# Kernel tuning notes

Measured on AMD Instinct MI355X. Metric: run time of the kernel, lower is better.

Reference implementation:

```python
import jax, jax.numpy as jnp
import numpy as np

HIDDEN = 1024
NUM_HEADS = 4
HEAD_DIM = HIDDEN // NUM_HEADS
SCALE = HEAD_DIM ** -0.5
EPS = 1e-5


def setup_inputs() -> dict:
    key = jax.random.key(0)
    ks = jax.random.split(key, 8)
    B, S, D = 4, 2048, HIDDEN
    x = jax.random.normal(ks[0], (B, S, D), dtype=jnp.float32)
    attention_mask = jnp.ones((B, S), dtype=jnp.int32)
    init = 1.0 / np.sqrt(D)
    Wq = jax.random.uniform(ks[1], (D, D), jnp.float32, -init, init)
    Wk = jax.random.uniform(ks[2], (D, D), jnp.float32, -init, init)
    Wv = jax.random.uniform(ks[3], (D, D), jnp.float32, -init, init)
    Wo = jax.random.uniform(ks[4], (D, D), jnp.float32, -init, init)
    bo = jax.random.uniform(ks[5], (D,), jnp.float32, -init, init)
    gamma = jnp.ones((D,), dtype=jnp.float32)
    beta = jnp.zeros((D,), dtype=jnp.float32)
    return {"x": x, "attention_mask": attention_mask, "Wq": Wq, "Wk": Wk,
            "Wv": Wv, "Wo": Wo, "bo": bo, "gamma": gamma, "beta": beta}


def reference(x, attention_mask, Wq, Wk, Wv, Wo, bo, gamma, beta):
    # Linear layers: y = x @ W^T (torch nn.Linear convention), no bias for q/k/v
    q = jnp.einsum('bsd,ed->bse', x, Wq)
    k = jnp.einsum('bsd,ed->bse', x, Wk)
    v = jnp.einsum('bsd,ed->bse', x, Wv)
    # Full-width attention (module never splits heads), scale = head_dim^-0.5
    scores = jnp.einsum('bqd,bkd->bqk', q, k) * SCALE  # [B,S,S]
    mask = attention_mask[:, None, :]  # [B,1,S]
    scores = jnp.where(mask == 0, jnp.float32(-1e9), scores)
    attn = jax.nn.softmax(scores, axis=-1)
    ctx = jnp.einsum('bqk,bkd->bqd', attn, v)
    out = jnp.einsum('bsd,ed->bse', ctx, Wo) + bo
    # residual + LayerNorm
    h = out + x
    mu = jnp.mean(h, axis=-1, keepdims=True)
    var = jnp.mean(jnp.square(h - mu), axis=-1, keepdims=True)
    return (h - mu) * jax.lax.rsqrt(var + EPS) * gamma + beta
```

## Files before the change

### kernel.cpp

```cpp
#include <hip/hip_runtime.h>

typedef __bf16 bf16;
typedef __bf16 bf16x8 __attribute__((ext_vector_type(8)));
typedef __bf16 bf16x4 __attribute__((ext_vector_type(4)));
typedef float floatx4 __attribute__((ext_vector_type(4)));

#define HIDDEN 1024
#define SEQ 2048
#define BATCH 4
#define ATT_SCALE 0.0625f
#define LN_EPS 1e-5f
#define WW (HIDDEN * HIDDEN)

__device__ __forceinline__ void gload_lds16(const void* g, void* l) {
    __builtin_amdgcn_global_load_lds(
        (const __attribute__((address_space(1))) unsigned int*)g,
        (__attribute__((address_space(3))) unsigned int*)l, 16, 0, 0);
}

#define GBAR() asm volatile("s_barrier" ::: "memory")
#define LGKM0() do { asm volatile("s_waitcnt lgkmcnt(0)" ::: "memory"); \
                     __builtin_amdgcn_sched_barrier(0); } while (0)
#define VMC(N) asm volatile("s_waitcnt vmcnt(" #N ")" ::: "memory")
#define MFMA(a, b, c) __builtin_amdgcn_mfma_f32_16x16x32_bf16(a, b, c, 0, 0, 0)

__global__ void cvt_f32_bf16(const float* __restrict__ in, bf16* __restrict__ out, int n4) {
    int i = blockIdx.x * blockDim.x + threadIdx.x;
    if (i >= n4) return;
    float4 v = ((const float4*)in)[i];
    bf16x4 o;
    o[0] = (bf16)v.x; o[1] = (bf16)v.y; o[2] = (bf16)v.z; o[3] = (bf16)v.w;
    ((bf16x4*)out)[i] = o;
}

__global__ void transpose_w3(const float* __restrict__ s0, const float* __restrict__ s1,
                             const float* __restrict__ s2,
                             bf16* __restrict__ d0p, bf16* __restrict__ d1p, bf16* __restrict__ d2p) {
    const float* in = (blockIdx.z == 0) ? s0 : (blockIdx.z == 1) ? s1 : s2;
    bf16* out = (blockIdx.z == 0) ? d0p : (blockIdx.z == 1) ? d1p : d2p;
    __shared__ __attribute__((aligned(16))) bf16 tile[64][72];
    const int d0 = blockIdx.x * 64;
    const int f0 = blockIdx.y * 64;
    const int t = threadIdx.x;
    const int r = t >> 4;
    const int c = (t & 15) * 4;
#pragma unroll
    for (int i = 0; i < 4; ++i) {
        float4 v = *(const float4*)&in[(long)(f0 + r + i * 16) * HIDDEN + d0 + c];
        bf16x4 b;
        b[0] = (bf16)v.x; b[1] = (bf16)v.y; b[2] = (bf16)v.z; b[3] = (bf16)v.w;
        *(bf16x4*)&tile[r + i * 16][c] = b;
    }
    __syncthreads();
#pragma unroll
    for (int i = 0; i < 4; ++i) {
        const int dr = r + i * 16;
        bf16x4 o;
#pragma unroll
        for (int j = 0; j < 4; ++j) o[j] = tile[c + j][dr];
        *(bf16x4*)&out[(long)(d0 + dr) * HIDDEN + f0 + c] = o;
    }
}

template <int MODE>
__global__ __launch_bounds__(512, 2)
void gemm8p(const bf16* A, const bf16* Bw, void* __restrict__ Cout,
            int lda, int ldb, int ldc, int K, float scale,
            long sA, long sB, long sC, int zmod) {
    __shared__ __attribute__((aligned(16))) char lds[131072];

    const int gx = gridDim.x;
    const int nblk = gx * gridDim.y;
    const int bid = blockIdx.y * gx + blockIdx.x;
    const int cpx = nblk >> 3;
    const int sbid = (nblk & 7) ? bid : (bid & 7) * cpx + (bid >> 3);
    const int bx = sbid % gx, by = sbid / gx;

    const int z = blockIdx.z;
    const int mat = z % zmod, ks = z / zmod;
    const char* Ab = (const char*)(A + (long)mat * sA + (long)ks * K);
    const char* Bb = (const char*)(Bw + (long)mat * sB + (long)ks * K);
    const long lda2 = lda * 2L, ldb2 = ldb * 2L;

    const int t = threadIdx.x;
    const int lane = t & 63;
    const int w = t >> 6;
    const int wm = w >> 2;
    const int wn = w & 3;
    const int l15 = lane & 15;
    const int l4 = lane >> 4;

    const int row0 = by * 256;
    const int col0 = bx * 256;

    const int sc = ((((t & 3) - ((t >> 3) & 3)) & 3) << 4);
    const char* aS[2];
    const char* bS[2];
#pragma unroll
    for (int uu = 0; uu < 2; ++uu) {
        aS[uu] = Ab + (long)(row0 + uu * 128 + (t >> 2)) * lda2 + sc;
        bS[uu] = Bb + (long)(col0 + uu * 128 + (t >> 2)) * ldb2 + sc;
    }

    auto STAGE = [&](char* dstu, const char* const* sp, long koff) {
        gload_lds16(sp[0] + koff, dstu + t * 16);
        gload_lds16(sp[1] + koff, dstu + 8192 + t * 16);
    };

    floatx4 acc[8][4] = {};
    const int nk = K / 64;

    STAGE(lds + 0,     aS, 0);
    STAGE(lds + 16384, bS, 0);
    STAGE(lds + 32768, aS, 64);
    STAGE(lds + 49152, bS, 64);
    VMC(4);
    GBAR();

    for (int tt = 0; tt < nk; ++tt) {
        const char* cb = lds + (tt & 1) * 65536;
        char* nb = lds + ((tt & 1) ^ 1) * 65536;
        const long nko = (long)((tt + 1 < nk) ? tt + 1 : nk - 1) * 128;

        auto RDA = [&](int kk, int m) {
            int lr = wm * 128 + m * 16 + l15;
            return *(const bf16x8*)(cb + kk * 32768 + lr * 64 + ((((lr >> 1) + l4) & 3) << 4));
        };
        auto RDB = [&](int kk, int n) {
            int lr = wn * 64 + n * 16 + l15;
            return *(const bf16x8*)(cb + 16384 + kk * 32768 + lr * 64 + ((((lr >> 1) + l4) & 3) << 4));
        };

        bf16x8 a[4], b0[4], b1[4];

#pragma unroll
        for (int m = 0; m < 4; ++m) a[m] = RDA(0, m);
#pragma unroll
        for (int n = 0; n < 4; ++n) b0[n] = RDB(0, n);
        STAGE(nb + 0, aS, nko);
        GBAR();
        LGKM0();
        __builtin_amdgcn_s_setprio(1);
#pragma unroll
        for (int m = 0; m < 4; ++m)
#pragma unroll
            for (int n = 0; n < 4; ++n) acc[m][n] = MFMA(a[m], b0[n], acc[m][n]);
        __builtin_amdgcn_s_setprio(0);
        GBAR();

#pragma unroll
        for (int m = 0; m < 4; ++m) a[m] = RDA(0, 4 + m);
        STAGE(nb + 16384, bS, nko);
        GBAR();
        LGKM0();
        __builtin_amdgcn_s_setprio(1);
#pragma unroll
        for (int m = 0; m < 4; ++m)
#pragma unroll
            for (int n = 0; n < 4; ++n) acc[4 + m][n] = MFMA(a[m], b0[n], acc[4 + m][n]);
        __builtin_amdgcn_s_setprio(0);
        VMC(4);
        GBAR();

#pragma unroll
        for (int m = 0; m < 4; ++m) a[m] = RDA(1, m);
#pragma unroll
        for (int n = 0; n < 4; ++n) b1[n] = RDB(1, n);
        STAGE(nb + 32768, aS, nko + 64);
        GBAR();
        LGKM0();
        __builtin_amdgcn_s_setprio(1);
#pragma unroll
        for (int m = 0; m < 4; ++m)
#pragma unroll
            for (int n = 0; n < 4; ++n) acc[m][n] = MFMA(a[m], b1[n], acc[m][n]);
        __builtin_amdgcn_s_setprio(0);
        GBAR();

#pragma unroll
        for (int m = 0; m < 4; ++m) a[m] = RDA(1, 4 + m);
        STAGE(nb + 49152, bS, nko + 64);
        GBAR();
        LGKM0();
        __builtin_amdgcn_s_setprio(1);
#pragma unroll
        for (int m = 0; m < 4; ++m)
#pragma unroll
            for (int n = 0; n < 4; ++n) acc[4 + m][n] = MFMA(a[m], b1[n], acc[4 + m][n]);
        __builtin_amdgcn_s_setprio(0);
        VMC(4);
        GBAR();
    }
    VMC(0);

    const int rq = l4 * 4;
    if constexpr (MODE == 0) {
        bf16* C = ((bf16*)Cout) + (long)z * sC;
#pragma unroll
        for (int m = 0; m < 8; ++m)
#pragma unroll
            for (int i = 0; i < 4; ++i) {
                long gr = row0 + wm * 128 + m * 16 + rq + i;
#pragma unroll
                for (int n = 0; n < 4; ++n) {
                    int gc = col0 + wn * 64 + n * 16 + l15;
                    C[gr * ldc + gc] = (bf16)(acc[m][n][i] * scale);
                }
            }
    } else {
        float* C = (float*)Cout + (long)z * sC;
#pragma unroll
        for (int m = 0; m < 8; ++m)
#pragma unroll
            for (int i = 0; i < 4; ++i) {
                long gr = row0 + wm * 128 + m * 16 + rq + i;
#pragma unroll
                for (int n = 0; n < 4; ++n) {
                    int gc = col0 + wn * 64 + n * 16 + l15;
                    C[gr * ldc + gc] = acc[m][n][i];
                }
            }
    }
}

__global__ void reduce_wgc(const float* __restrict__ p, bf16* __restrict__ out) {
    int i = blockIdx.x * blockDim.x + threadIdx.x;
    int e = i * 4;
    int mat = e >> 20;
    int local = e & (WW - 1);
    float4 s = *(const float4*)(p + (long)mat * WW + local);
#pragma unroll
    for (int ksp = 1; ksp < 4; ++ksp) {
        float4 a = *(const float4*)(p + (long)(ksp * 2 + mat) * WW + local);
        s.x += a.x; s.y += a.y; s.z += a.z; s.w += a.w;
    }
    bf16x4 o;
    o[0] = (bf16)s.x; o[1] = (bf16)s.y; o[2] = (bf16)s.z; o[3] = (bf16)s.w;
    *(bf16x4*)&out[e] = o;
}

__global__ void softmax_rows(bf16* __restrict__ S, const int* __restrict__ mask) {
    const int b = blockIdx.y;
    const int row = blockIdx.x;
    bf16* srow = S + ((long)b * SEQ + row) * SEQ;
    const int* mrow = mask + b * SEQ;
    const int t = threadIdx.x;

    bf16x8 sv = *(const bf16x8*)&srow[t * 8];
    int4 m0 = ((const int4*)mrow)[t * 2];
    int4 m1 = ((const int4*)mrow)[t * 2 + 1];
    int mk[8] = {m0.x, m0.y, m0.z, m0.w, m1.x, m1.y, m1.z, m1.w};

    float v[8];
    float mx = -1e30f;
#pragma unroll
    for (int j = 0; j < 8; ++j) {
        float s = (float)sv[j];
        if (mk[j] == 0) s = -1e9f;
        v[j] = s;
        mx = fmaxf(mx, s);
    }
    __shared__ float redm[4], reds[4];
#pragma unroll
    for (int off = 32; off > 0; off >>= 1) mx = fmaxf(mx, __shfl_down(mx, off));
    if ((t & 63) == 0) redm[t >> 6] = mx;
    __syncthreads();
    mx = fmaxf(fmaxf(redm[0], redm[1]), fmaxf(redm[2], redm[3]));

    float sum = 0.f;
#pragma unroll
    for (int j = 0; j < 8; ++j) {
        v[j] = __expf(v[j] - mx);
        sum += v[j];
    }
#pragma unroll
    for (int off = 32; off > 0; off >>= 1) sum += __shfl_down(sum, off);
    if ((t & 63) == 0) reds[t >> 6] = sum;
    __syncthreads();
    sum = reds[0] + reds[1] + reds[2] + reds[3];
    float inv = 1.0f / sum;

    bf16x8 o;
#pragma unroll
    for (int j = 0; j < 8; ++j) o[j] = (bf16)(v[j] * inv);
    *(bf16x8*)&srow[t * 8] = o;
}

__global__ void transpose_v(const bf16* __restrict__ yv, bf16* __restrict__ out) {
    __shared__ __attribute__((aligned(16))) bf16 tile[64][72];
    const int z = blockIdx.z;
    const bf16* ib = yv + (long)z * SEQ * 2048 + 1024;
    bf16* ob = out + (long)z * SEQ * HIDDEN;
    const int d0 = blockIdx.x * 64;
    const int s0 = blockIdx.y * 64;
    const int t = threadIdx.x;
    const int r = t >> 4;
    const int c = (t & 15) * 4;
#pragma unroll
    for (int i = 0; i < 4; ++i) {
        bf16x4 v = *(const bf16x4*)&ib[(long)(s0 + r + i * 16) * 2048 + d0 + c];
        *(bf16x4*)&tile[r + i * 16][c] = v;
    }
    __syncthreads();
#pragma unroll
    for (int i = 0; i < 4; ++i) {
        const int dr = r + i * 16;
        bf16x4 o;
#pragma unroll
        for (int j = 0; j < 4; ++j) o[j] = tile[c + j][dr];
        *(bf16x4*)&ob[(long)(d0 + dr) * SEQ + s0 + c] = o;
    }
}

__global__ void layernorm_out(const bf16* __restrict__ pp, const float* __restrict__ x,
                              const float* __restrict__ bo, const float* __restrict__ gamma,
                              const float* __restrict__ beta, float* __restrict__ out) {
    const long row = blockIdx.x;
    const int b = (int)(row >> 11);
    const int s = (int)(row & 2047);
    const bf16* r0 = pp + ((long)b * SEQ + s) * HIDDEN;
    const bf16* r1 = r0 + 4L * SEQ * HIDDEN;
    const int t = threadIdx.x;

    bf16x4 a0 = ((const bf16x4*)r0)[t];
    bf16x4 a1 = ((const bf16x4*)r1)[t];
    float4 xv = ((const float4*)(x + row * HIDDEN))[t];
    float4 bv = ((const float4*)bo)[t];
    float4 v;
    v.x = (float)a0[0] + (float)a1[0] + bv.x + xv.x;
    v.y = (float)a0[1] + (float)a1[1] + bv.y + xv.y;
    v.z = (float)a0[2] + (float)a1[2] + bv.z + xv.z;
    v.w = (float)a0[3] + (float)a1[3] + bv.w + xv.w;

    float ssum = v.x + v.y + v.z + v.w;
    float sq = v.x * v.x + v.y * v.y + v.z * v.z + v.w * v.w;
    __shared__ float rs[4], rq[4];
#pragma unroll
    for (int off = 32; off > 0; off >>= 1) {
        ssum += __shfl_down(ssum, off);
        sq += __shfl_down(sq, off);
    }
    if ((t & 63) == 0) { rs[t >> 6] = ssum; rq[t >> 6] = sq; }
    __syncthreads();
    ssum = rs[0] + rs[1] + rs[2] + rs[3];
    sq = rq[0] + rq[1] + rq[2] + rq[3];
    float mu = ssum * (1.0f / HIDDEN);
    float var = sq * (1.0f / HIDDEN) - mu * mu;
    float rinv = rsqrtf(var + LN_EPS);
    float4 g = ((const float4*)gamma)[t];
    float4 bt = ((const float4*)beta)[t];
    float4 o;
    o.x = (v.x - mu) * rinv * g.x + bt.x;
    o.y = (v.y - mu) * rinv * g.y + bt.y;
    o.z = (v.z - mu) * rinv * g.z + bt.z;
    o.w = (v.w - mu) * rinv * g.w + bt.w;
    ((float4*)(out + row * HIDDEN))[t] = o;
}

extern "C" void kernel_launch(void* const* d_in, const int* in_sizes, int n_in,
                              void* d_out, int out_size, void* d_ws, size_t ws_size,
                              hipStream_t stream) {
    const float* x     = (const float*)d_in[0];
    const int*   mask  = (const int*)d_in[1];
    const float* Wq    = (const float*)d_in[2];
    const float* Wk    = (const float*)d_in[3];
    const float* Wv    = (const float*)d_in[4];
    const float* Wo    = (const float*)d_in[5];
    const float* bo    = (const float*)d_in[6];
    const float* gamma = (const float*)d_in[7];
    const float* beta  = (const float*)d_in[8];
    float* out = (float*)d_out;

    char* ws = (char*)d_ws;
    const long MB = 1024L * 1024L;
    bf16* yv   = (bf16*)(ws + 0 * MB);
    bf16* pp   = (bf16*)(ws + 0 * MB);
    bf16* xb   = (bf16*)(ws + 32 * MB);
    bf16* vt   = (bf16*)(ws + 48 * MB);
    bf16* wgc  = (bf16*)(ws + 64 * MB);
    bf16* wkT  = (bf16*)(ws + 68 * MB);
    bf16* wo   = (bf16*)(ws + 70 * MB);
    bf16* wqT  = (bf16*)(ws + 72 * MB);
    bf16* wvT  = (bf16*)(ws + 74 * MB);
    bf16* S    = (bf16*)(ws + 76 * MB);
    float* wgcp = (float*)(ws + 76 * MB);

    const int BS = BATCH * SEQ;
    dim3 blk256(256), blk512(512);

    cvt_f32_bf16<<<dim3(BS * HIDDEN / 4 / 256), blk256, 0, stream>>>(x, xb, BS * HIDDEN / 4);
    cvt_f32_bf16<<<dim3(WW / 4 / 256), blk256, 0, stream>>>(Wo, wo, WW / 4);
    transpose_w3<<<dim3(16, 16, 3), blk256, 0, stream>>>(Wq, Wk, Wv, wqT, wkT, wvT);

    gemm8p<4><<<dim3(1024 / 256, 1024 / 256, 8), blk512, 0, stream>>>(
        wkT, wqT, wgcp, HIDDEN, HIDDEN, HIDDEN, 256, 1.0f,
        (long)WW, (long)WW, (long)WW, 2);
    reduce_wgc<<<dim3(2 * WW / 4 / 256), blk256, 0, stream>>>(wgcp, wgc);

    gemm8p<0><<<dim3(2048 / 256, BS / 256, 1), blk512, 0, stream>>>(
        xb, wgc, yv, HIDDEN, HIDDEN, 2048, HIDDEN, 1.0f, 0, 0, 0, 1);

    transpose_v<<<dim3(HIDDEN / 64, SEQ / 64, BATCH), blk256, 0, stream>>>(yv, vt);

    gemm8p<0><<<dim3(SEQ / 256, SEQ / 256, BATCH), blk512, 0, stream>>>(
        yv, xb, S, 2048, HIDDEN, SEQ, HIDDEN, ATT_SCALE,
        (long)SEQ * 2048, (long)SEQ * HIDDEN, (long)SEQ * SEQ, 4);

    softmax_rows<<<dim3(SEQ, BATCH), blk256, 0, stream>>>(S, mask);

    gemm8p<0><<<dim3(HIDDEN / 256, SEQ / 256, 8), blk512, 0, stream>>>(
        S, vt, pp, SEQ, SEQ, HIDDEN, 1024, 1.0f,
        (long)SEQ * SEQ, (long)HIDDEN * SEQ, (long)SEQ * HIDDEN, 4);

    layernorm_out<<<dim3(BS), blk256, 0, stream>>>(pp, x, bo, gamma, beta, out);
}
```

Baseline: 186.8 us.

## Restructure GEMM mainloop into a four-slot K32 ring with one barrier per step

```diff
diff --git a/kernel.cpp b/kernel.cpp
--- a/kernel.cpp
+++ b/kernel.cpp
@@ -19,8 +19,6 @@
 }
 
 #define GBAR() asm volatile("s_barrier" ::: "memory")
-#define LGKM0() do { asm volatile("s_waitcnt lgkmcnt(0)" ::: "memory"); \
-                     __builtin_amdgcn_sched_barrier(0); } while (0)
 #define VMC(N) asm volatile("s_waitcnt vmcnt(" #N ")" ::: "memory")
 #define MFMA(a, b, c) __builtin_amdgcn_mfma_f32_16x16x32_bf16(a, b, c, 0, 0, 0)
 
@@ -63,10 +61,10 @@
 }
 
 template <int MODE>
-__global__ __launch_bounds__(512, 2)
-void gemm8p(const bf16* A, const bf16* Bw, void* __restrict__ Cout,
-            int lda, int ldb, int ldc, int K, float scale,
-            long sA, long sB, long sC, int zmod) {
+__global__ __launch_bounds__(512, 1)
+void gemmk32(const bf16* A, const bf16* Bw, void* __restrict__ Cout,
+             int lda, int ldb, int ldc, int K, float scale,
+             long sA, long sB, long sC, int zmod) {
     __shared__ __attribute__((aligned(16))) char lds[131072];
 
     const int gx = gridDim.x;
@@ -102,92 +100,48 @@
         bS[uu] = Bb + (long)(col0 + uu * 128 + (t >> 2)) * ldb2 + sc;
     }
 
-    auto STAGE = [&](char* dstu, const char* const* sp, long koff) {
-        gload_lds16(sp[0] + koff, dstu + t * 16);
-        gload_lds16(sp[1] + koff, dstu + 8192 + t * 16);
+    auto STAGE = [&](int ring, long koff) {
+        char* base = lds + ring * 32768;
+        gload_lds16(aS[0] + koff, base + t * 16);
+        gload_lds16(aS[1] + koff, base + 8192 + t * 16);
+        gload_lds16(bS[0] + koff, base + 16384 + t * 16);
+        gload_lds16(bS[1] + koff, base + 24576 + t * 16);
     };
 
     floatx4 acc[8][4] = {};
-    const int nk = K / 64;
-
-    STAGE(lds + 0,     aS, 0);
-    STAGE(lds + 16384, bS, 0);
-    STAGE(lds + 32768, aS, 64);
-    STAGE(lds + 49152, bS, 64);
+    const int ns = K / 32;
+
+    STAGE(0, 0);
+    STAGE(1, 64);
     VMC(4);
     GBAR();
 
-    for (int tt = 0; tt < nk; ++tt) {
-        const char* cb = lds + (tt & 1) * 65536;
-        char* nb = lds + ((tt & 1) ^ 1) * 65536;
-        const long nko = (long)((tt + 1 < nk) ? tt + 1 : nk - 1) * 128;
-
-        auto RDA = [&](int kk, int m) {
+    for (int s = 0; s < ns; ++s) {
+        const char* sb = lds + (s & 3) * 32768;
+
+        const long pko = (long)((s + 2 < ns) ? s + 2 : ns - 1) * 64;
+        STAGE((s + 2) & 3, pko);
+
+        bf16x8 a[8], b[4];
+#pragma unroll
+        for (int n = 0; n < 4; ++n) {
+            int lr = wn * 64 + n * 16 + l15;
+            b[n] = *(const bf16x8*)(sb + 16384 + lr * 64 + ((((lr >> 1) + l4) & 3) << 4));
+        }
+#pragma unroll
+        for (int m = 0; m < 8; ++m) {
             int lr = wm * 128 + m * 16 + l15;
-            return *(const bf16x8*)(cb + kk * 32768 + lr * 64 + ((((lr >> 1) + l4) & 3) << 4));
-        };
-        auto RDB = [&](int kk, int n) {
-            int lr = wn * 64 + n * 16 + l15;
-            return *(const bf16x8*)(cb + 16384 + kk * 32768 + lr * 64 + ((((lr >> 1) + l4) & 3) << 4));
-        };
-
-        bf16x8 a[4], b0[4], b1[4];
-
-#pragma unroll
-        for (int m = 0; m < 4; ++m) a[m] = RDA(0, m);
-#pragma unroll
-        for (int n = 0; n < 4; ++n) b0[n] = RDB(0, n);
-        STAGE(nb + 0, aS, nko);
-        GBAR();
-        LGKM0();
+            a[m] = *(const bf16x8*)(sb + lr * 64 + ((((lr >> 1) + l4) & 3) << 4));
+        }
+
         __builtin_amdgcn_s_setprio(1);
 #pragma unroll
-        for (int m = 0; m < 4; ++m)
-#pragma unroll
-            for (int n = 0; n < 4; ++n) acc[m][n] = MFMA(a[m], b0[n], acc[m][n]);
+        for (int m = 0; m < 8; ++m)
+#pragma unroll
+            for (int n = 0; n < 4; ++n)
+                acc[m][n] = MFMA(a[m], b[n], acc[m][n]);
         __builtin_amdgcn_s_setprio(0);
-        GBAR();
-
-#pragma unroll
-        for (int m = 0; m < 4; ++m) a[m] = RDA(0, 4 + m);
-        STAGE(nb + 16384, bS, nko);
-        GBAR();
-        LGKM0();
-        __builtin_amdgcn_s_setprio(1);
-#pragma unroll
-        for (int m = 0; m < 4; ++m)
-#pragma unroll
-            for (int n = 0; n < 4; ++n) acc[4 + m][n] = MFMA(a[m], b0[n], acc[4 + m][n]);
-        __builtin_amdgcn_s_setprio(0);
-        VMC(4);
-        GBAR();
-
-#pragma unroll
-        for (int m = 0; m < 4; ++m) a[m] = RDA(1, m);
-#pragma unroll
-        for (int n = 0; n < 4; ++n) b1[n] = RDB(1, n);
-        STAGE(nb + 32768, aS, nko + 64);
-        GBAR();
-        LGKM0();
-        __builtin_amdgcn_s_setprio(1);
-#pragma unroll
-        for (int m = 0; m < 4; ++m)
-#pragma unroll
-            for (int n = 0; n < 4; ++n) acc[m][n] = MFMA(a[m], b1[n], acc[m][n]);
-        __builtin_amdgcn_s_setprio(0);
-        GBAR();
-
-#pragma unroll
-        for (int m = 0; m < 4; ++m) a[m] = RDA(1, 4 + m);
-        STAGE(nb + 49152, bS, nko + 64);
-        GBAR();
-        LGKM0();
-        __builtin_amdgcn_s_setprio(1);
-#pragma unroll
-        for (int m = 0; m < 4; ++m)
-#pragma unroll
-            for (int n = 0; n < 4; ++n) acc[4 + m][n] = MFMA(a[m], b1[n], acc[4 + m][n]);
-        __builtin_amdgcn_s_setprio(0);
+
         VMC(4);
         GBAR();
     }
@@ -392,23 +346,23 @@
     cvt_f32_bf16<<<dim3(WW / 4 / 256), blk256, 0, stream>>>(Wo, wo, WW / 4);
     transpose_w3<<<dim3(16, 16, 3), blk256, 0, stream>>>(Wq, Wk, Wv, wqT, wkT, wvT);
 
-    gemm8p<4><<<dim3(1024 / 256, 1024 / 256, 8), blk512, 0, stream>>>(
+    gemmk32<4><<<dim3(1024 / 256, 1024 / 256, 8), blk512, 0, stream>>>(
         wkT, wqT, wgcp, HIDDEN, HIDDEN, HIDDEN, 256, 1.0f,
         (long)WW, (long)WW, (long)WW, 2);
     reduce_wgc<<<dim3(2 * WW / 4 / 256), blk256, 0, stream>>>(wgcp, wgc);
 
-    gemm8p<0><<<dim3(2048 / 256, BS / 256, 1), blk512, 0, stream>>>(
+    gemmk32<0><<<dim3(2048 / 256, BS / 256, 1), blk512, 0, stream>>>(
         xb, wgc, yv, HIDDEN, HIDDEN, 2048, HIDDEN, 1.0f, 0, 0, 0, 1);
 
     transpose_v<<<dim3(HIDDEN / 64, SEQ / 64, BATCH), blk256, 0, stream>>>(yv, vt);
 
-    gemm8p<0><<<dim3(SEQ / 256, SEQ / 256, BATCH), blk512, 0, stream>>>(
+    gemmk32<0><<<dim3(SEQ / 256, SEQ / 256, BATCH), blk512, 0, stream>>>(
         yv, xb, S, 2048, HIDDEN, SEQ, HIDDEN, ATT_SCALE,
         (long)SEQ * 2048, (long)SEQ * HIDDEN, (long)SEQ * SEQ, 4);
 
     softmax_rows<<<dim3(SEQ, BATCH), blk256, 0, stream>>>(S, mask);
 
-    gemm8p<0><<<dim3(HIDDEN / 256, SEQ / 256, 8), blk512, 0, stream>>>(
+    gemmk32<0><<<dim3(HIDDEN / 256, SEQ / 256, 8), blk512, 0, stream>>>(
         S, vt, pp, SEQ, SEQ, HIDDEN, 1024, 1.0f,
         (long)SEQ * SEQ, (long)HIDDEN * SEQ, (long)SEQ * HIDDEN, 4);
 
```

After: 187.0 us. Within noise of the previous version (+0.1%).
